# Optimization experiments

Hardware: AMD Instinct MI355X
Metric: run time of the kernel (lower is better)

Reference implementation:

```python
import jax, jax.numpy as jnp
import jax.scipy.linalg as jsl
import numpy as np

EPS = 1e-7            # torchvision iou-loss eps
GIOU_THRESHOLD = 0.2
MIN_VARIANCE = 1e-6


def cxcywh_to_xyxy(b):
    cx, cy, w, h = b[..., 0], b[..., 1], b[..., 2], b[..., 3]
    return jnp.stack([cx - 0.5 * w, cy - 0.5 * h, cx + 0.5 * w, cy + 0.5 * h], axis=-1)


def kalman_filtered_boxes(prev_boxes, prev_logits, image_sizes, swp, sws, log_q_diag):
    # scale: [B,1,4] = [w,h,w,h] for denormalization
    scale = jnp.stack([image_sizes[:, 1], image_sizes[:, 0], image_sizes[:, 1], image_sizes[:, 0]], axis=-1)[:, None, :]
    box_abs = prev_boxes * scale                               # [B,Q,4] absolute cxcywh
    conf = jax.nn.softmax(prev_logits, axis=-1).max(axis=-1)   # [B,Q]
    # predict step: P_pred = F P0 F^T + Q  (track-independent 8x8)
    idx = jnp.arange(4)
    F = jnp.eye(8, dtype=box_abs.dtype).at[idx, idx + 4].set(1.0)
    P0 = jnp.diag(jnp.array([100.0] * 4 + [1000.0] * 4, dtype=box_abs.dtype))
    Qm = jnp.diag(jnp.exp(log_q_diag))
    P_pred = F @ P0 @ F.T + Qm                                 # [8,8]
    # detection covariance R per track (DetectionCovarianceGate)
    hc = jnp.maximum(box_abs[..., 3], 1.0)
    std = jnp.stack([swp * hc, swp * hc, sws * hc, sws * hc], axis=-1)
    std = std / jnp.maximum(conf, 1e-6)[..., None]
    std = jnp.maximum(std, 0.1)
    eye4 = jnp.eye(4, dtype=box_abs.dtype)
    R = eye4 * (std ** 2)[..., None, :] + MIN_VARIANCE * eye4  # [B,Q,4,4]
    # innovation covariance, gain via batched Cholesky + triangular solves
    S = P_pred[:4, :4] + R + MIN_VARIANCE * eye4               # [B,Q,4,4]
    L = jnp.linalg.cholesky(S)
    covHT_T = jnp.broadcast_to(P_pred[:, :4].T, S.shape[:-2] + (4, 8))
    y = jsl.solve_triangular(L, covHT_T, lower=True)
    Kt = jsl.solve_triangular(jnp.swapaxes(L, -1, -2), y, lower=False)
    K = jnp.swapaxes(Kt, -1, -2)                               # [B,Q,8,4]
    # state init from the same box + zero velocity -> F @ mean0 = [box; 0]
    mean_pred = jnp.concatenate([box_abs, jnp.zeros_like(box_abs)], axis=-1)  # [B,Q,8]
    innovation = box_abs - mean_pred[..., :4]  # identically zero; kept faithful to original
    mean_new = mean_pred + jnp.einsum('bqij,bqj->bqi', K, innovation)
    return mean_new[..., :4] / scale


def pairwise_giou_loss(p, t):
    # p: [B,Q,4], t: [B,T,4] in xyxy -> [B,Q,T] GIoU loss
    a = p[:, :, None, :]
    b = t[:, None, :, :]
    area_a = (a[..., 2] - a[..., 0]) * (a[..., 3] - a[..., 1])
    area_b = (b[..., 2] - b[..., 0]) * (b[..., 3] - b[..., 1])
    lt = jnp.maximum(a[..., :2], b[..., :2])
    rb = jnp.minimum(a[..., 2:], b[..., 2:])
    wh = jnp.maximum(rb - lt, 0.0)
    inter = wh[..., 0] * wh[..., 1]
    union = area_a + area_b - inter
    iou = inter / (union + EPS)
    ltc = jnp.minimum(a[..., :2], b[..., :2])
    rbc = jnp.maximum(a[..., 2:], b[..., 2:])
    whc = jnp.maximum(rbc - ltc, 0.0)
    area_c = whc[..., 0] * whc[..., 1]
    giou = iou - (area_c - union) / (area_c + EPS)
    return 1.0 - giou


def ciou_loss_mean(p, t):
    # elementwise complete-IoU loss (torchvision semantics), mean-reduced
    x1, y1, x2, y2 = p[..., 0], p[..., 1], p[..., 2], p[..., 3]
    xg1, yg1, xg2, yg2 = t[..., 0], t[..., 1], t[..., 2], t[..., 3]
    iw = jnp.maximum(jnp.minimum(x2, xg2) - jnp.maximum(x1, xg1), 0.0)
    ih = jnp.maximum(jnp.minimum(y2, yg2) - jnp.maximum(y1, yg1), 0.0)
    inter = iw * ih
    union = (x2 - x1) * (y2 - y1) + (xg2 - xg1) * (yg2 - yg1) - inter
    iou = inter / (union + EPS)
    cw = jnp.maximum(x2, xg2) - jnp.minimum(x1, xg1)
    ch = jnp.maximum(y2, yg2) - jnp.minimum(y1, yg1)
    c2 = cw ** 2 + ch ** 2 + EPS
    d2 = ((x1 + x2 - xg1 - xg2) ** 2 + (y1 + y2 - yg1 - yg2) ** 2) / 4.0
    v = (4.0 / (jnp.pi ** 2)) * (jnp.arctan((xg2 - xg1) / (yg2 - yg1)) - jnp.arctan((x2 - x1) / (y2 - y1))) ** 2
    alpha = jax.lax.stop_gradient(v / (1.0 - iou + v + EPS))
    return jnp.mean(1.0 - iou + d2 / c2 + alpha * v)


def _hungarian(cost):
    # O(n^3) shortest-augmenting-path Hungarian (min-cost square assignment).
    # Returns col assignment for rows 0..n-1 (rows are implicitly arange(n)).
    n = cost.shape[0]
    u = np.zeros(n + 1)
    v = np.zeros(n + 1)
    p = np.zeros(n + 1, dtype=np.int64)
    way = np.zeros(n + 1, dtype=np.int64)
    for i in range(1, n + 1):
        p[0] = i
        j0 = 0
        minv = np.full(n + 1, np.inf)
        used = np.zeros(n + 1, dtype=bool)
        while True:
            used[j0] = True
            i0 = p[j0]
            js = np.nonzero(~used)[0]
            js = js[js > 0]
            cur = cost[i0 - 1, js - 1] - u[i0] - v[js]
            upd = cur < minv[js]
            minv[js] = np.minimum(minv[js], cur)
            way[js[upd]] = j0
            j1 = js[int(np.argmin(minv[js]))]
            delta = minv[j1]
            uj = np.nonzero(used)[0]
            u[p[uj]] += delta
            v[uj] -= delta
            minv[js] -= delta
            j0 = j1
            if p[j0] == 0:
                break
        while j0 != 0:
            j1 = way[j0]
            p[j0] = p[j1]
            j0 = j1
    col_of_row = np.empty(n, dtype=np.int64)
    for j in range(1, n + 1):
        col_of_row[p[j] - 1] = j - 1
    return col_of_row


def setup_inputs() -> dict:
    key = jax.random.key(0)
    k = jax.random.split(key, 4)
    B, Q, C = 8, 512, 92
    prev_boxes = jax.random.uniform(k[0], (B, Q, 4), jnp.float32)
    prev_logits = jax.random.normal(k[1], (B, Q, C), jnp.float32)
    curr_boxes = jax.random.uniform(k[2], (B, Q, 4), jnp.float32)
    image_sizes = jax.random.uniform(k[3], (B, 2), jnp.float32) * 800.0 + 480.0
    return {
        'prev_boxes': prev_boxes,
        'prev_logits': prev_logits,
        'curr_boxes': curr_boxes,
        'image_sizes': image_sizes,
        'std_weight_position': jnp.asarray(0.05, jnp.float32),
        'std_weight_size': jnp.asarray(0.05, jnp.float32),
        'log_q_diag': jnp.log(jnp.array([0.01] * 4 + [1e-4] * 4, jnp.float32)),
    }


def reference(prev_boxes, prev_logits, curr_boxes, image_sizes, std_weight_position, std_weight_size, log_q_diag):
    filtered = kalman_filtered_boxes(prev_boxes, prev_logits, image_sizes,
                                     std_weight_position, std_weight_size, log_q_diag)
    # Hungarian matching on thresholded pairwise GIoU-loss cost (no-grad in original)
    gl = pairwise_giou_loss(cxcywh_to_xyxy(curr_boxes), cxcywh_to_xyxy(filtered))  # [B,Q,Q]
    cost = np.asarray(jax.lax.stop_gradient(gl) < GIOU_THRESHOLD, dtype=np.float64)
    cols = jnp.asarray(np.stack([_hungarian(cost[b]) for b in range(cost.shape[0])]))
    # original: matched_preds = pred[col_indices]; matched_targets = target[row_indices] (rows=arange)
    matched_preds = jnp.take_along_axis(curr_boxes, cols[..., None], axis=1)
    matched_targets = filtered
    return ciou_loss_mean(cxcywh_to_xyxy(matched_preds), cxcywh_to_xyxy(matched_targets))
```

## Files before the change

### kernel.cpp

```cpp
#include <hip/hip_runtime.h>
#include <stdint.h>
#include <math.h>

#define NB 8
#define NQ 512

typedef unsigned long long u64;

#define CW(k, r) costL[((k) << 9) + (r)]

static __device__ __forceinline__ u64 getw8(const u64 (&a)[8], int w) {
    u64 r = 0ull;
#pragma unroll
    for (int k = 0; k < 8; k++) if (k == w) r = a[k];
    return r;
}
static __device__ __forceinline__ void setbit8(u64 (&a)[8], int c) {
    int w = c >> 6; u64 m = 1ull << (c & 63);
#pragma unroll
    for (int k = 0; k < 8; k++) if (k == w) a[k] |= m;
}
static __device__ __forceinline__ bool getbit8(const u64 (&a)[8], int c) {
    return (getw8(a, c >> 6) >> (c & 63)) & 1ull;
}

__global__ void prep_kernel(const float* __restrict__ prev_boxes,
                            const float* __restrict__ image_sizes,
                            float4* __restrict__ filt,
                            float* __restrict__ out) {
#pragma clang fp contract(off)
    int t = blockIdx.x * blockDim.x + threadIdx.x;
    if (t == 0) out[0] = 0.f;
    int b = t >> 9;
    float4 pb = ((const float4*)prev_boxes)[t];
    float H = image_sizes[2 * b + 0];
    float W = image_sizes[2 * b + 1];
    float fcx = (pb.x * W) / W, fcy = (pb.y * H) / H;
    float fw  = (pb.z * W) / W, fh  = (pb.w * H) / H;
    filt[t] = make_float4(fcx - 0.5f * fw, fcy - 0.5f * fh,
                          fcx + 0.5f * fw, fcy + 0.5f * fh);
}

__global__ void cost_kernel(const float* __restrict__ curr_boxes,
                            const float4* __restrict__ filt,
                            u64* __restrict__ cost) {
#pragma clang fp contract(off)
    int t = blockIdx.x * blockDim.x + threadIdx.x;
    int b = t >> 18;
    int rem = t & (NQ * NQ - 1);
    int i = rem >> 9;
    int j = rem & (NQ - 1);
    float4 cb = ((const float4*)curr_boxes)[(b << 9) + i];
    float ax = cb.x - 0.5f * cb.z, ay = cb.y - 0.5f * cb.w;
    float az = cb.x + 0.5f * cb.z, aw = cb.y + 0.5f * cb.w;
    float4 fb = filt[(b << 9) + j];
    float bx = fb.x, by = fb.y, bz = fb.z, bw = fb.w;
    float area_a = (az - ax) * (aw - ay);
    float area_b = (bz - bx) * (bw - by);
    float ltx = fmaxf(ax, bx), lty = fmaxf(ay, by);
    float rbx = fminf(az, bz), rby = fminf(aw, bw);
    float w = fmaxf(rbx - ltx, 0.f), h = fmaxf(rby - lty, 0.f);
    float inter = w * h;
    float uni = area_a + area_b - inter;
    float iou = inter / (uni + 1e-7f);
    float lcx = fminf(ax, bx), lcy = fminf(ay, by);
    float rcx = fmaxf(az, bz), rcy = fmaxf(aw, bw);
    float wc = fmaxf(rcx - lcx, 0.f), hc = fmaxf(rcy - lcy, 0.f);
    float areac = wc * hc;
    float giou = iou - (areac - uni) / (areac + 1e-7f);
    float gl = 1.f - giou;
    u64 m = __ballot(gl < 0.2f);
    if ((threadIdx.x & 63) == 0)
        cost[(size_t)b * (NQ * 8) + ((size_t)(j >> 6) << 9) + i] = m;
}

__global__ __launch_bounds__(256, 1) void hungarian_kernel(
        const u64* __restrict__ cost,
        const float* __restrict__ curr_boxes,
        const float4* __restrict__ filt,
        float* __restrict__ out) {
    int b = blockIdx.x;
    int tid = threadIdx.x;
    int lane = tid & 63;
    int wv = tid >> 6;
    __shared__ __align__(16) u64 costL[NQ * 8];
    __shared__ int p[NQ + 1];
    __shared__ int wayL[NQ + 1];
    __shared__ int u[NQ + 1];
    __shared__ int vv[NQ + 1];
    __shared__ int minvA[NQ + 1];
    __shared__ unsigned char used[NQ + 1];

    {
        const ulonglong2* src = (const ulonglong2*)(cost + (size_t)b * NQ * 8);
        ulonglong2* dst = (ulonglong2*)costL;
        for (int k = tid; k < NQ * 4; k += 256) dst[k] = src[k];
    }
    for (int k = tid; k <= NQ; k += 256) { p[k] = k; wayL[k] = 0; u[k] = 0; vv[k] = 0; }
    __syncthreads();

    if (wv == 0) {
        auto runGeneral = [&](int igen) {
            for (int j = igen; j <= NQ; j++) p[j] = 0;
            for (int i2 = igen; i2 <= NQ; i2++) {
                p[0] = i2;
                for (int j = 0; j <= NQ; j++) { minvA[j] = 0x7fffffff; used[j] = 0; }
                int j0 = 0;
                while (true) {
                    used[j0] = 1;
                    int i0 = p[j0];
                    int ui0 = u[i0];
                    int delta = 0x7fffffff, j1 = 0;
                    for (int j = 1; j <= NQ; j++) {
                        if (!used[j]) {
                            int cbit = (int)((CW((j - 1) >> 6, i0 - 1) >> ((j - 1) & 63)) & 1ull);
                            int cur = cbit - ui0 - vv[j];
                            if (cur < minvA[j]) { minvA[j] = cur; wayL[j] = (i2 << 10) | j0; }
                            if (minvA[j] < delta) { delta = minvA[j]; j1 = j; }
                        }
                    }
                    for (int j = 0; j <= NQ; j++) {
                        if (used[j]) { u[p[j]] += delta; vv[j] -= delta; }
                        else minvA[j] -= delta;
                    }
                    j0 = j1;
                    if (p[j0] == 0) break;
                }
                while (j0) {
                    int wv2 = wayL[j0];
                    int jn = ((wv2 >> 10) == i2) ? (wv2 & 1023) : 0;
                    p[j0] = p[jn];
                    j0 = jn;
                }
            }
        };

        u64 Zc[8];
#pragma unroll
        for (int k = 0; k < 8; k++) Zc[k] = 0ull;
        int owner0 = 1;
        bool done = false;

        for (int g = 0; g < 8 && !done; g++) {
            u64 R[8];
            int r = (g << 6) + lane;
#pragma unroll
            for (int k = 0; k < 8; k++) R[k] = CW(k, r);
            u64 orR = 0ull;
#pragma unroll
            for (int k = 0; k < 8; k++) orR |= R[k];
            u64 nzw = __ballot(orR != 0ull);
            u64 c0w = __ballot((R[0] & 1ull) != 0ull);
            u64 dgw = __ballot(((getw8(R, g) >> lane) & 1ull) != 0ull);

            if (g == 0) {
                if ((nzw & c0w) & 1ull) {
                    if (lane == 0) runGeneral(1);
                    done = true;
                    break;
                }
#pragma unroll
                for (int k = 0; k < 8; k++) Zc[k] = CW(k, 0);
            }
            u64 ao = 0ull;
#pragma unroll
            for (int k = 0; k < 8; k++) ao |= (R[k] & Zc[k]);
            u64 apw = __ballot(ao != 0ull);
            u64 bits = nzw & (c0w | dgw | apw);
            if (g == 0) bits &= ~1ull;

            while (bits) {
                int l = __builtin_ctzll(bits);
                u64 rem = (l == 63) ? 0ull : (~0ull << (l + 1));
                int i = (g << 6) + l + 1;
                bool c0 = (c0w >> l) & 1ull;
                bool apb = (apw >> l) & 1ull;
                if (!c0 && !apb) {
                    if (lane == 0) { p[i] = owner0; p[1] = i; }
                    owner0 = i;
#pragma unroll
                    for (int k = 0; k < 8; k++) Zc[k] = CW(k, i - 1);
                } else {
                    bool bail = false, hole = false;
                    u64 Z[8];
#pragma unroll
                    for (int k = 0; k < 8; k++) Z[k] = CW(k, i - 1);
                    u64 ones[8], vis[8], nzA[8], nzBf[8];
#pragma unroll
                    for (int k = 0; k < 8; k++) { ones[k] = Z[k]; vis[k] = 0ull; nzA[k] = 0ull; nzBf[k] = 0ull; }
                    int fA_c = 0, fA_p = 0, fB_c = 0, fB_p = 0;
                    int foldn = 0, assignTo = -1;
                    while (true) {
                        int c2 = -1;
#pragma unroll
                        for (int k = 7; k >= 0; k--) {
                            u64 s = ~ones[k] & ~vis[k];
                            if (s != 0ull) c2 = (k << 6) + __builtin_ctzll(s);
                        }
                        if (c2 < 0) { bail = true; break; }
                        if (c2 >= i - 1) {
                            if (c2 == i - 1) assignTo = c2;
                            else hole = true;
                            break;
                        }
                        int pc = p[c2 + 1];
                        u64 Zo[8];
#pragma unroll
                        for (int k = 0; k < 8; k++) Zo[k] = CW(k, pc - 1);
                        setbit8(vis, c2);
                        u64 nzv[8], ap2 = 0ull;
#pragma unroll
                        for (int k = 0; k < 8; k++) { nzv[k] = ones[k] & ~Zo[k]; ones[k] &= Zo[k]; ap2 |= ones[k]; }
                        if (foldn == 0) {
                            fA_c = c2; fA_p = pc;
#pragma unroll
                            for (int k = 0; k < 8; k++) nzA[k] = nzv[k];
                        } else if (foldn == 1) {
                            fB_c = c2; fB_p = pc;
#pragma unroll
                            for (int k = 0; k < 8; k++) nzBf[k] = nzv[k];
                        } else {
                            if (lane == 0) {
#pragma unroll
                                for (int k = 0; k < 8; k++) {
                                    u64 tt = nzv[k];
                                    while (tt) { int b2 = __builtin_ctzll(tt); tt &= tt - 1; wayL[(k << 6) + b2 + 1] = (i << 10) | (c2 + 1); }
                                }
                            }
                        }
                        foldn++;
                        if (ap2 == 0ull) { assignTo = i - 1; break; }
                    }
                    if (bail || hole) {
                        if (lane == 0) runGeneral(i);
                        done = true;
                        break;
                    }
                    int cc = assignTo;
                    while (true) {
                        bool inA = getbit8(nzA, cc), inB = getbit8(nzBf, cc);
                        if (inB)      { if (lane == 0) p[cc + 1] = fB_p; cc = fB_c; }
                        else if (inA) { if (lane == 0) p[cc + 1] = fA_p; cc = fA_c; }
                        else if (foldn > 2) {
                            int wv2 = wayL[cc + 1];
                            if ((wv2 >> 10) == i) { int jn = wv2 & 1023; int pv = p[jn]; if (lane == 0) p[cc + 1] = pv; cc = jn - 1; }
                            else                  { if (lane == 0) p[cc + 1] = i; break; }
                        } else { if (lane == 0) p[cc + 1] = i; break; }
                    }
                    owner0 = p[1];
#pragma unroll
                    for (int k = 0; k < 8; k++) Zc[k] = CW(k, owner0 - 1);
                }
                u64 ao2 = 0ull;
#pragma unroll
                for (int k = 0; k < 8; k++) ao2 |= (R[k] & Zc[k]);
                apw = __ballot(ao2 != 0ull);
                bits = nzw & (c0w | dgw | apw) & rem;
            }
        }
    }
    __syncthreads();

    {
#pragma clang fp contract(off)
        float sum = 0.f;
#pragma unroll
        for (int k = 0; k < 2; k++) {
            int j = 1 + tid + (k << 8);
            int r = p[j] - 1;
            int c = j - 1;
            float4 cb = ((const float4*)curr_boxes)[(b << 9) + c];
            float x1 = cb.x - 0.5f * cb.z, y1 = cb.y - 0.5f * cb.w;
            float x2 = cb.x + 0.5f * cb.z, y2 = cb.y + 0.5f * cb.w;
            float4 fb = filt[(b << 9) + r];
            float xg1 = fb.x, yg1 = fb.y, xg2 = fb.z, yg2 = fb.w;
            float iw = fmaxf(fminf(x2, xg2) - fmaxf(x1, xg1), 0.f);
            float ih = fmaxf(fminf(y2, yg2) - fmaxf(y1, yg1), 0.f);
            float inter = iw * ih;
            float uni = (x2 - x1) * (y2 - y1) + (xg2 - xg1) * (yg2 - yg1) - inter;
            float iou = inter / (uni + 1e-7f);
            float cw2 = fmaxf(x2, xg2) - fminf(x1, xg1);
            float ch2 = fmaxf(y2, yg2) - fminf(y1, yg1);
            float c2 = cw2 * cw2 + ch2 * ch2 + 1e-7f;
            float dx = ((x1 + x2) - xg1) - xg2;
            float dy = ((y1 + y2) - yg1) - yg2;
            float d2 = (dx * dx + dy * dy) / 4.f;
            const float CC = (float)(4.0 / (M_PI * M_PI));
            float at = atanf((xg2 - xg1) / (yg2 - yg1)) - atanf((x2 - x1) / (y2 - y1));
            float v = CC * (at * at);
            float alpha = v / (((1.f - iou) + v) + 1e-7f);
            sum += ((1.f - iou) + d2 / c2) + alpha * v;
        }
#pragma unroll
        for (int off = 32; off >= 1; off >>= 1) sum += __shfl_xor(sum, off, 64);
        if (lane == 0) atomicAdd(out, sum * (1.f / 4096.f));
    }
}

extern "C" void kernel_launch(void* const* d_in, const int* in_sizes, int n_in,
                              void* d_out, int out_size, void* d_ws, size_t ws_size,
                              hipStream_t stream) {
    const float* prev_boxes  = (const float*)d_in[0];
    const float* curr_boxes  = (const float*)d_in[2];
    const float* image_sizes = (const float*)d_in[3];

    float4* filt = (float4*)d_ws;
    u64* cost = (u64*)((char*)d_ws + 65536);
    float* out = (float*)d_out;

    prep_kernel<<<(NB * NQ) / 256, 256, 0, stream>>>(
        prev_boxes, image_sizes, filt, out);
    cost_kernel<<<(NB * NQ * NQ) / 256, 256, 0, stream>>>(
        curr_boxes, filt, cost);
    hungarian_kernel<<<NB, 256, 0, stream>>>(
        cost, curr_boxes, filt, out);
}
```

Measured before the change: 77.72 us.

## Overlap CIoU prep with Hungarian solve on idle waves; coarsen cost kernel

While wave 0 runs the serial Hungarian solve, the other three waves now stage filtered and current boxes into shared memory and precompute the per-box atan terms, so the final CIoU pass reads LDS instead of global memory and skips the atan calls. The cost kernel now handles four pairs per thread with a quarter of the blocks, and the cost-matrix copy into LDS is fully unrolled. The intent is to hide the epilogue work behind the latency-bound matching loop and cut launch and wave overhead in the cost pass. It adds about 20KB of shared memory to a one-block-per-CU kernel.

```diff
diff --git a/kernel.cpp b/kernel.cpp
--- a/kernel.cpp
+++ b/kernel.cpp
@@ -45,33 +45,37 @@
                             const float4* __restrict__ filt,
                             u64* __restrict__ cost) {
 #pragma clang fp contract(off)
-    int t = blockIdx.x * blockDim.x + threadIdx.x;
-    int b = t >> 18;
-    int rem = t & (NQ * NQ - 1);
-    int i = rem >> 9;
-    int j = rem & (NQ - 1);
-    float4 cb = ((const float4*)curr_boxes)[(b << 9) + i];
-    float ax = cb.x - 0.5f * cb.z, ay = cb.y - 0.5f * cb.w;
-    float az = cb.x + 0.5f * cb.z, aw = cb.y + 0.5f * cb.w;
-    float4 fb = filt[(b << 9) + j];
-    float bx = fb.x, by = fb.y, bz = fb.z, bw = fb.w;
-    float area_a = (az - ax) * (aw - ay);
-    float area_b = (bz - bx) * (bw - by);
-    float ltx = fmaxf(ax, bx), lty = fmaxf(ay, by);
-    float rbx = fminf(az, bz), rby = fminf(aw, bw);
-    float w = fmaxf(rbx - ltx, 0.f), h = fmaxf(rby - lty, 0.f);
-    float inter = w * h;
-    float uni = area_a + area_b - inter;
-    float iou = inter / (uni + 1e-7f);
-    float lcx = fminf(ax, bx), lcy = fminf(ay, by);
-    float rcx = fmaxf(az, bz), rcy = fmaxf(aw, bw);
-    float wc = fmaxf(rcx - lcx, 0.f), hc = fmaxf(rcy - lcy, 0.f);
-    float areac = wc * hc;
-    float giou = iou - (areac - uni) / (areac + 1e-7f);
-    float gl = 1.f - giou;
-    u64 m = __ballot(gl < 0.2f);
-    if ((threadIdx.x & 63) == 0)
-        cost[(size_t)b * (NQ * 8) + ((size_t)(j >> 6) << 9) + i] = m;
+    int t0 = blockIdx.x * blockDim.x + threadIdx.x;
+#pragma unroll
+    for (int rep = 0; rep < 4; rep++) {
+        int t = t0 + rep * (NB * NQ * NQ / 4);
+        int b = t >> 18;
+        int rem = t & (NQ * NQ - 1);
+        int i = rem >> 9;
+        int j = rem & (NQ - 1);
+        float4 cb = ((const float4*)curr_boxes)[(b << 9) + i];
+        float ax = cb.x - 0.5f * cb.z, ay = cb.y - 0.5f * cb.w;
+        float az = cb.x + 0.5f * cb.z, aw = cb.y + 0.5f * cb.w;
+        float4 fb = filt[(b << 9) + j];
+        float bx = fb.x, by = fb.y, bz = fb.z, bw = fb.w;
+        float area_a = (az - ax) * (aw - ay);
+        float area_b = (bz - bx) * (bw - by);
+        float ltx = fmaxf(ax, bx), lty = fmaxf(ay, by);
+        float rbx = fminf(az, bz), rby = fminf(aw, bw);
+        float w = fmaxf(rbx - ltx, 0.f), h = fmaxf(rby - lty, 0.f);
+        float inter = w * h;
+        float uni = area_a + area_b - inter;
+        float iou = inter / (uni + 1e-7f);
+        float lcx = fminf(ax, bx), lcy = fminf(ay, by);
+        float rcx = fmaxf(az, bz), rcy = fmaxf(aw, bw);
+        float wc = fmaxf(rcx - lcx, 0.f), hc = fmaxf(rcy - lcy, 0.f);
+        float areac = wc * hc;
+        float giou = iou - (areac - uni) / (areac + 1e-7f);
+        float gl = 1.f - giou;
+        u64 m = __ballot(gl < 0.2f);
+        if ((threadIdx.x & 63) == 0)
+            cost[(size_t)b * (NQ * 8) + ((size_t)(j >> 6) << 9) + i] = m;
+    }
 }
 
 __global__ __launch_bounds__(256, 1) void hungarian_kernel(
@@ -90,11 +94,19 @@
     __shared__ int vv[NQ + 1];
     __shared__ int minvA[NQ + 1];
     __shared__ unsigned char used[NQ + 1];
+    __shared__ __align__(16) float4 fbL[NQ];
+    __shared__ __align__(16) float4 cbL[NQ];
+    __shared__ float atF[NQ];
+    __shared__ float atC[NQ];
 
     {
         const ulonglong2* src = (const ulonglong2*)(cost + (size_t)b * NQ * 8);
         ulonglong2* dst = (ulonglong2*)costL;
-        for (int k = tid; k < NQ * 4; k += 256) dst[k] = src[k];
+#pragma unroll
+        for (int it = 0; it < 8; it++) {
+            int k = tid + (it << 8);
+            dst[k] = src[k];
+        }
     }
     for (int k = tid; k <= NQ; k += 256) { p[k] = k; wayL[k] = 0; u[k] = 0; vv[k] = 0; }
     __syncthreads();
@@ -258,6 +270,20 @@
                 bits = nzw & (c0w | dgw | apw) & rem;
             }
         }
+    } else {
+#pragma clang fp contract(off)
+        int q = tid - 64;
+        for (int r = q; r < NQ; r += 192) {
+            float4 fb = filt[(b << 9) + r];
+            fbL[r] = fb;
+            float xg1 = fb.x, yg1 = fb.y, xg2 = fb.z, yg2 = fb.w;
+            atF[r] = atanf((xg2 - xg1) / (yg2 - yg1));
+            float4 cbv = ((const float4*)curr_boxes)[(b << 9) + r];
+            cbL[r] = cbv;
+            float x1 = cbv.x - 0.5f * cbv.z, y1 = cbv.y - 0.5f * cbv.w;
+            float x2 = cbv.x + 0.5f * cbv.z, y2 = cbv.y + 0.5f * cbv.w;
+            atC[r] = atanf((x2 - x1) / (y2 - y1));
+        }
     }
     __syncthreads();
 
@@ -269,10 +295,10 @@
             int j = 1 + tid + (k << 8);
             int r = p[j] - 1;
             int c = j - 1;
-            float4 cb = ((const float4*)curr_boxes)[(b << 9) + c];
+            float4 cb = cbL[c];
             float x1 = cb.x - 0.5f * cb.z, y1 = cb.y - 0.5f * cb.w;
             float x2 = cb.x + 0.5f * cb.z, y2 = cb.y + 0.5f * cb.w;
-            float4 fb = filt[(b << 9) + r];
+            float4 fb = fbL[r];
             float xg1 = fb.x, yg1 = fb.y, xg2 = fb.z, yg2 = fb.w;
             float iw = fmaxf(fminf(x2, xg2) - fmaxf(x1, xg1), 0.f);
             float ih = fmaxf(fminf(y2, yg2) - fmaxf(y1, yg1), 0.f);
@@ -286,7 +312,7 @@
             float dy = ((y1 + y2) - yg1) - yg2;
             float d2 = (dx * dx + dy * dy) / 4.f;
             const float CC = (float)(4.0 / (M_PI * M_PI));
-            float at = atanf((xg2 - xg1) / (yg2 - yg1)) - atanf((x2 - x1) / (y2 - y1));
+            float at = atF[r] - atC[c];
             float v = CC * (at * at);
             float alpha = v / (((1.f - iou) + v) + 1e-7f);
             sum += ((1.f - iou) + d2 / c2) + alpha * v;
@@ -310,7 +336,7 @@
 
     prep_kernel<<<(NB * NQ) / 256, 256, 0, stream>>>(
         prev_boxes, image_sizes, filt, out);
-    cost_kernel<<<(NB * NQ * NQ) / 256, 256, 0, stream>>>(
+    cost_kernel<<<(NB * NQ * NQ / 4) / 256, 256, 0, stream>>>(
         curr_boxes, filt, cost);
     hungarian_kernel<<<NB, 256, 0, stream>>>(
         cost, curr_boxes, filt, out);
```

Result: no change. 77.70 us (-0.0%).
